# Performance work log

Measured on AMD Instinct MI355X. Metric: run time of the kernel, lower is better.

The kernel has to match this reference:

```python
import jax, jax.numpy as jnp
import numpy as np

D_MODEL, D_HIDDEN, D_OUTPUT = 512, 1024, 128

def setup_inputs() -> dict:
    key = jax.random.key(0)
    ks = jax.random.split(key, 6)
    enc = jax.random.normal(ks[0], (8, 256, D_MODEL), dtype=jnp.float32)
    dec = jax.random.normal(ks[1], (8, 64, D_MODEL), dtype=jnp.float32)
    s1 = 1.0 / np.sqrt(2 * D_MODEL)
    s2 = 1.0 / np.sqrt(D_HIDDEN)
    W1 = jax.random.uniform(ks[2], (2 * D_MODEL, D_HIDDEN), jnp.float32, -s1, s1)
    b1 = jax.random.uniform(ks[3], (D_HIDDEN,), jnp.float32, -s1, s1)
    W2 = jax.random.uniform(ks[4], (D_HIDDEN, D_OUTPUT), jnp.float32, -s2, s2)
    b2 = jax.random.uniform(ks[5], (D_OUTPUT,), jnp.float32, -s2, s2)
    return {"encoder_state": enc, "decoder_state": dec, "W1": W1, "b1": b1, "W2": W2, "b2": b2}

def reference(encoder_state, decoder_state, W1, b1, W2, b2):
    # Split first linear's weight into encoder/decoder halves: equivalent to
    # concat([enc, dec], -1) @ W1, but avoids materializing the (B,T,U,2d) tensor.
    W_enc, W_dec = W1[:D_MODEL], W1[D_MODEL:]
    enc_proj = jnp.einsum('btd,dh->bth', encoder_state, W_enc)   # (B,T,H)
    dec_proj = jnp.einsum('bud,dh->buh', decoder_state, W_dec)   # (B,U,H)
    hidden = jnp.tanh(enc_proj[:, :, None, :] + dec_proj[:, None, :, :] + b1)  # (B,T,U,H)
    out = jnp.einsum('btuh,ho->btuo', hidden, W2) + b2           # (B,T,U,O)
    return out
```

## Files before the change

### kernel.cpp

```cpp
#include <hip/hip_runtime.h>
#include <hip/hip_bf16.h>


typedef _Float16 f16x8 __attribute__((ext_vector_type(8)));
typedef _Float16 f16x2 __attribute__((ext_vector_type(2)));
typedef float    f32x4 __attribute__((ext_vector_type(4)));

#define C2L 2.8853900817779268f

__device__ __forceinline__ float fast_exp2(float x) { return __builtin_amdgcn_exp2f(x); }

__device__ __forceinline__ f16x2 pk_cvt(float x, float y) {
    auto r = __builtin_amdgcn_cvt_pkrtz(x, y);
    union { decltype(r) a; f16x2 b; } c; c.a = r; return c.b;
}

__device__ __forceinline__ f16x8 tanh8(f16x8 e, f16x8 d) {
    const f16x8 one = {1,1,1,1,1,1,1,1};
    const f16x8 two = {2,2,2,2,2,2,2,2};
    const f16x8 cap = {126,126,126,126,126,126,126,126};
    union { f16x8 v; _Float16 s[8]; } p, r;
    p.v = e * d + one;
    p.v = __builtin_elementwise_min(p.v, cap);
    #pragma unroll
    for (int i = 0; i < 4; ++i) {
        _Float16 q  = p.s[2*i] * p.s[2*i+1];
        _Float16 rq = __builtin_amdgcn_rcph(q);
        r.s[2*i]   = p.s[2*i+1] * rq;
        r.s[2*i+1] = p.s[2*i]   * rq;
    }
    return one - two * r.v;
}

__device__ __forceinline__ void stage16(const void* g, void* l) {
    __builtin_amdgcn_global_load_lds(
        (const __attribute__((address_space(1))) unsigned int*)g,
        (__attribute__((address_space(3))) unsigned int*)l, 16, 0, 0);
}

__global__ __launch_bounds__(1024) void transpose_both(
    const float* __restrict__ W1, const float* __restrict__ W2,
    _Float16* __restrict__ W1T, _Float16* __restrict__ W2T)
{
    __shared__ float tile[32][33];
    int bx = blockIdx.x;
    const float* src; _Float16* dst; int C, c0;
    if (bx < 32) { src = W1; dst = W1T; C = 1024; c0 = bx * 32; }
    else         { src = W2; dst = W2T; C = 128;  c0 = (bx - 32) * 32; }
    int r0 = blockIdx.y * 32;
    int tx = threadIdx.x, ty = threadIdx.y;
    tile[ty][tx] = src[(r0 + ty) * C + (c0 + tx)];
    __syncthreads();
    dst[(size_t)(c0 + ty) * 1024 + (r0 + tx)] = (_Float16)tile[tx][ty];
}

__global__ __launch_bounds__(256) void proj_exp(
    const float* __restrict__ enc,
    const float* __restrict__ dec,
    const _Float16* __restrict__ W1T,
    const float* __restrict__ b1,
    _Float16* __restrict__ Ep,
    _Float16* __restrict__ Dp)
{
    const int K = 512;
    int tid  = threadIdx.x;
    int w    = tid >> 6, lane = tid & 63;
    int quad = lane >> 4, l15 = lane & 15;
    int m_base = blockIdx.y * 64 + w * 16;
    int n_base = blockIdx.x * 64;

    bool is_enc = (m_base < 2048);
    const float* A = is_enc ? (enc + (size_t)(m_base + l15) * K)
                            : (dec + (size_t)(m_base - 2048 + l15) * K);
    int koff = is_enc ? 0 : 512;

    f32x4 acc[4] = {};
    for (int kc = 0; kc < K; kc += 32) {
        int k = kc + quad * 8;
        float4 a_lo = *reinterpret_cast<const float4*>(A + k);
        float4 a_hi = *reinterpret_cast<const float4*>(A + k + 4);
        union { f16x8 v; f16x2 h[4]; } a;
        a.h[0] = pk_cvt(a_lo.x, a_lo.y);
        a.h[1] = pk_cvt(a_lo.z, a_lo.w);
        a.h[2] = pk_cvt(a_hi.x, a_hi.y);
        a.h[3] = pk_cvt(a_hi.z, a_hi.w);
        #pragma unroll
        for (int f = 0; f < 4; ++f) {
            int n = n_base + f * 16 + l15;
            f16x8 b = *reinterpret_cast<const f16x8*>(W1T + n * 1024 + koff + k);
            acc[f] = __builtin_amdgcn_mfma_f32_16x16x32_f16(a.v, b, acc[f], 0, 0, 0);
        }
    }

    #pragma unroll
    for (int f = 0; f < 4; ++f) {
        int col = n_base + f * 16 + l15;
        float bv = is_enc ? b1[col] : 0.0f;
        #pragma unroll
        for (int v = 0; v < 4; ++v) {
            int row = m_base + quad * 4 + v;
            float val = fast_exp2(C2L * (acc[f][v] + bv));
            if (is_enc) Ep[(size_t)row * 1024 + col] = (_Float16)val;
            else        Dp[(size_t)(row - 2048) * 1024 + col] = (_Float16)val;
        }
    }
}

__global__ __launch_bounds__(256, 4) void joint_main(
    const _Float16* __restrict__ Ep,
    const _Float16* __restrict__ Dp,
    const _Float16* __restrict__ W2T,
    const float* __restrict__ b2,
    float* __restrict__ out)
{
    __shared__ _Float16 sB[2][128 * 64];

    int t0 = blockIdx.x * 2, b = blockIdx.y;
    int tid  = threadIdx.x;
    int w    = tid >> 6, lane = tid & 63;
    int quad = lane >> 4, l15 = lane & 15;
    int u0   = w * 16;

    const _Float16* ep0 = Ep + (size_t)(b * 256 + t0) * 1024;
    const _Float16* ep1 = ep0 + 1024;
    const _Float16* dpr = Dp + (size_t)(b * 64 + u0 + l15) * 1024;

    f32x4 acc0[8] = {}, acc1[8] = {};

    #pragma unroll
    for (int i = 0; i < 4; ++i) {
        int c = i * 256 + tid;
        int row = c >> 3, kcs = c & 7;
        stage16(W2T + row * 1024 + ((kcs ^ (row & 7)) << 3),
                &sB[0][(i * 256 + (tid & 0xC0)) * 8]);
    }

    for (int it = 0; it < 16; ++it) {
        __syncthreads();
        if (it < 15) {
            int kb = (it + 1) * 64;
            _Float16* dst = sB[(it + 1) & 1];
            #pragma unroll
            for (int i = 0; i < 4; ++i) {
                int c = i * 256 + tid;
                int row = c >> 3, kcs = c & 7;
                stage16(W2T + row * 1024 + kb + ((kcs ^ (row & 7)) << 3),
                        dst + (i * 256 + (tid & 0xC0)) * 8);
            }
        }
        const _Float16* sb = sB[it & 1];
        #pragma unroll
        for (int ki2 = 0; ki2 < 2; ++ki2) {
            int k = it * 64 + ki2 * 32 + quad * 8;
            f16x8 d8 = *reinterpret_cast<const f16x8*>(dpr + k);
            f16x8 e0 = *reinterpret_cast<const f16x8*>(ep0 + k);
            f16x8 e1 = *reinterpret_cast<const f16x8*>(ep1 + k);
            f16x8 A0 = tanh8(e0, d8);
            f16x8 A1 = tanh8(e1, d8);
            int kc3 = ki2 * 4 + quad;
            int sw  = (kc3 ^ (l15 & 7)) << 3;
            #pragma unroll
            for (int f = 0; f < 8; ++f) {
                f16x8 bb = *reinterpret_cast<const f16x8*>(
                    sb + (f * 16 + l15) * 64 + sw);
                acc0[f] = __builtin_amdgcn_mfma_f32_16x16x32_f16(A0, bb, acc0[f], 0, 0, 0);
                acc1[f] = __builtin_amdgcn_mfma_f32_16x16x32_f16(A1, bb, acc1[f], 0, 0, 0);
            }
        }
    }

    float* o0 = out + (size_t)(b * 256 + t0) * 64 * 128;
    float* o1 = o0 + 64 * 128;
    #pragma unroll
    for (int f = 0; f < 8; ++f) {
        int o = f * 16 + l15;
        float bv = b2[o];
        #pragma unroll
        for (int v = 0; v < 4; ++v) {
            int u = u0 + quad * 4 + v;
            o0[u * 128 + o] = acc0[f][v] + bv;
            o1[u * 128 + o] = acc1[f][v] + bv;
        }
    }
}

extern "C" void kernel_launch(void* const* d_in, const int* in_sizes, int n_in,
                              void* d_out, int out_size, void* d_ws, size_t ws_size,
                              hipStream_t stream) {
    const float* enc = (const float*)d_in[0];
    const float* dec = (const float*)d_in[1];
    const float* W1  = (const float*)d_in[2];
    const float* b1  = (const float*)d_in[3];
    const float* W2  = (const float*)d_in[4];
    const float* b2  = (const float*)d_in[5];
    float* out = (float*)d_out;

    char* ws = (char*)d_ws;
    _Float16* W1T = (_Float16*)(ws);
    _Float16* W2T = (_Float16*)(ws + (2u << 20));
    _Float16* EpP = (_Float16*)(ws + (2u << 20) + (256u << 10));
    _Float16* DpP = (_Float16*)(ws + (6u << 20) + (256u << 10));

    transpose_both<<<dim3(36, 32), dim3(32, 32), 0, stream>>>(W1, W2, W1T, W2T);

    proj_exp<<<dim3(16, 40), 256, 0, stream>>>(enc, dec, W1T, b1, EpP, DpP);

    joint_main<<<dim3(128, 8), 256, 0, stream>>>(EpP, DpP, W2T, b2, out);
}
```

Measured before the change: 160.9 us.

## Process four encoder timesteps per block with encoder rows staged in LDS

Each joint_main block now handles four t positions instead of two, so every W2 tile loaded from LDS feeds four MFMAs instead of two and the W2 staging cost is spread over more work. The four encoder rows are loaded into shared memory once at kernel start, replacing per-iteration global reads. The cost is 128 accumulator registers per thread, so the occupancy hint is lowered to 2 blocks per CU. The grid is halved to 512 blocks, which risks lower latency hiding and poorer load balance across CUs.

Result: faster. 155.9 us (-3.1%).

```diff
diff --git a/kernel.cpp b/kernel.cpp
--- a/kernel.cpp
+++ b/kernel.cpp
@@ -106,7 +106,7 @@
     }
 }
 
-__global__ __launch_bounds__(256, 4) void joint_main(
+__global__ __launch_bounds__(256, 2) void joint_main(
     const _Float16* __restrict__ Ep,
     const _Float16* __restrict__ Dp,
     const _Float16* __restrict__ W2T,
@@ -114,19 +114,24 @@
     float* __restrict__ out)
 {
     __shared__ _Float16 sB[2][128 * 64];
-
-    int t0 = blockIdx.x * 2, b = blockIdx.y;
+    __shared__ _Float16 sE[4 * 1024];
+
+    int t0 = blockIdx.x * 4, b = blockIdx.y;
     int tid  = threadIdx.x;
     int w    = tid >> 6, lane = tid & 63;
     int quad = lane >> 4, l15 = lane & 15;
     int u0   = w * 16;
 
-    const _Float16* ep0 = Ep + (size_t)(b * 256 + t0) * 1024;
-    const _Float16* ep1 = ep0 + 1024;
+    const _Float16* epB = Ep + (size_t)(b * 256 + t0) * 1024;
     const _Float16* dpr = Dp + (size_t)(b * 64 + u0 + l15) * 1024;
 
-    f32x4 acc0[8] = {}, acc1[8] = {};
-
+    f32x4 acc[4][8] = {};
+
+    #pragma unroll
+    for (int i = 0; i < 2; ++i) {
+        int c = i * 256 + tid;
+        stage16(epB + c * 8, sE + (i * 256 + (tid & 0xC0)) * 8);
+    }
     #pragma unroll
     for (int i = 0; i < 4; ++i) {
         int c = i * 256 + tid;
@@ -153,33 +158,37 @@
         for (int ki2 = 0; ki2 < 2; ++ki2) {
             int k = it * 64 + ki2 * 32 + quad * 8;
             f16x8 d8 = *reinterpret_cast<const f16x8*>(dpr + k);
-            f16x8 e0 = *reinterpret_cast<const f16x8*>(ep0 + k);
-            f16x8 e1 = *reinterpret_cast<const f16x8*>(ep1 + k);
-            f16x8 A0 = tanh8(e0, d8);
-            f16x8 A1 = tanh8(e1, d8);
+            f16x8 A[4];
+            #pragma unroll
+            for (int tt = 0; tt < 4; ++tt) {
+                f16x8 e = *reinterpret_cast<const f16x8*>(sE + tt * 1024 + k);
+                A[tt] = tanh8(e, d8);
+            }
             int kc3 = ki2 * 4 + quad;
             int sw  = (kc3 ^ (l15 & 7)) << 3;
             #pragma unroll
             for (int f = 0; f < 8; ++f) {
                 f16x8 bb = *reinterpret_cast<const f16x8*>(
                     sb + (f * 16 + l15) * 64 + sw);
-                acc0[f] = __builtin_amdgcn_mfma_f32_16x16x32_f16(A0, bb, acc0[f], 0, 0, 0);
-                acc1[f] = __builtin_amdgcn_mfma_f32_16x16x32_f16(A1, bb, acc1[f], 0, 0, 0);
-            }
-        }
-    }
-
-    float* o0 = out + (size_t)(b * 256 + t0) * 64 * 128;
-    float* o1 = o0 + 64 * 128;
-    #pragma unroll
-    for (int f = 0; f < 8; ++f) {
-        int o = f * 16 + l15;
-        float bv = b2[o];
-        #pragma unroll
-        for (int v = 0; v < 4; ++v) {
-            int u = u0 + quad * 4 + v;
-            o0[u * 128 + o] = acc0[f][v] + bv;
-            o1[u * 128 + o] = acc1[f][v] + bv;
+                #pragma unroll
+                for (int tt = 0; tt < 4; ++tt)
+                    acc[tt][f] = __builtin_amdgcn_mfma_f32_16x16x32_f16(A[tt], bb, acc[tt][f], 0, 0, 0);
+            }
+        }
+    }
+
+    #pragma unroll
+    for (int tt = 0; tt < 4; ++tt) {
+        float* o = out + (size_t)(b * 256 + t0 + tt) * 64 * 128;
+        #pragma unroll
+        for (int f = 0; f < 8; ++f) {
+            int oc = f * 16 + l15;
+            float bv = b2[oc];
+            #pragma unroll
+            for (int v = 0; v < 4; ++v) {
+                int u = u0 + quad * 4 + v;
+                o[u * 128 + oc] = acc[tt][f][v] + bv;
+            }
         }
     }
 }
@@ -205,5 +214,5 @@
 
     proj_exp<<<dim3(16, 40), 256, 0, stream>>>(enc, dec, W1T, b1, EpP, DpP);
 
-    joint_main<<<dim3(128, 8), 256, 0, stream>>>(EpP, DpP, W2T, b2, out);
-}
+    joint_main<<<dim3(64, 8), 256, 0, stream>>>(EpP, DpP, W2T, b2, out);
+}
```
